# Optimization experiments

Hardware: AMD Instinct MI355X
Metric: run time of the kernel (lower is better)

Reference implementation:

```python
import jax, jax.numpy as jnp
import numpy as np

N_NODES = 100000
N_EDGES = 600000
N_GRAPHS = 64
EPS = 1e-5


def setup_inputs() -> dict:
    key = jax.random.key(0)
    ks = jax.random.split(key, 8)
    x = jax.random.normal(ks[0], (N_NODES, 128), dtype=jnp.float32)
    edge_index = jax.random.randint(ks[1], (2, N_EDGES), 0, N_NODES, dtype=jnp.int64)
    batch = jnp.sort(jax.random.randint(ks[2], (N_NODES,), 0, N_GRAPHS, dtype=jnp.int64))
    conv_w = jax.random.normal(ks[3], (6, 128, 128), dtype=jnp.float32) * (1.0 / np.sqrt(128))
    conv_b = jnp.zeros((6, 128), dtype=jnp.float32)
    bn_g = jnp.ones((6, 128), dtype=jnp.float32)
    bn_b = jnp.zeros((6, 128), dtype=jnp.float32)
    lin1_w = jax.random.normal(ks[4], (128, 64), dtype=jnp.float32) * (1.0 / np.sqrt(128))
    lin1_b = jnp.zeros((64,), dtype=jnp.float32)
    lin2_w = jax.random.normal(ks[5], (64, 4), dtype=jnp.float32) * (1.0 / np.sqrt(64))
    lin2_b = jnp.zeros((4,), dtype=jnp.float32)
    return {"x": x, "edge_index": edge_index, "batch": batch,
            "conv_w": conv_w, "conv_b": conv_b, "bn_g": bn_g, "bn_b": bn_b,
            "lin1_w": lin1_w, "lin1_b": lin1_b, "lin2_w": lin2_w, "lin2_b": lin2_b}


def reference(x, edge_index, batch, conv_w, conv_b, bn_g, bn_b, lin1_w, lin1_b, lin2_w, lin2_b):
    src, dst = edge_index[0], edge_index[1]  # messages flow src -> dst (PyG source_to_target)
    n = x.shape[0]
    h = x
    # 6 stacked GCNConv(normalize=False) -> ReLU -> BatchNorm1d (training-mode batch stats)
    for i in range(6):
        m = h @ conv_w[i]                                   # [N, H] transform first
        agg = jax.ops.segment_sum(m[src], dst, num_segments=n) + conv_b[i]
        h = jax.nn.relu(agg)
        mean = h.mean(axis=0)
        var = h.var(axis=0)                                  # biased, matches torch BN
        h = (h - mean) * jax.lax.rsqrt(var + EPS) * bn_g[i] + bn_b[i]
    # global mean pool over graphs
    s = jax.ops.segment_sum(h, batch, num_segments=N_GRAPHS)          # [G, H]
    cnt = jax.ops.segment_sum(jnp.ones((n,), h.dtype), batch, num_segments=N_GRAPHS)
    pooled = s / jnp.maximum(cnt, 1.0)[:, None]
    out = pooled @ lin1_w + lin1_b
    out = out @ lin2_w + lin2_b
    return jax.nn.log_softmax(out, axis=-1)
```

## Files before the change

kernel.cpp:

```cpp
#include <hip/hip_runtime.h>
#include <math.h>

#define NN 100000
#define NE 600000
#define NG 64
#define HD 128
#define NL 6
#define NB 1563
#define PSL 16
#define ASTR 136

typedef unsigned short ushort_t;
typedef short short8 __attribute__((ext_vector_type(8)));
typedef float floatx4 __attribute__((ext_vector_type(4)));

__device__ __forceinline__ float bf2f(ushort_t u) {
    return __uint_as_float(((unsigned)u) << 16);
}
__device__ __forceinline__ ushort_t f2bf(float f) {
    unsigned u = __float_as_uint(f);
    unsigned r = (u + 0x7fffu + ((u >> 16) & 1u)) >> 16;
    return (ushort_t)r;
}


__global__ __launch_bounds__(256) void k_cast(const float* __restrict__ x,
                                              ushort_t* __restrict__ xb) {
    int i = blockIdx.x * 256 + threadIdx.x;
    if (i < NN * 32) {
        float4 v = ((const float4*)x)[i];
        ((ushort4*)xb)[i] = make_ushort4(f2bf(v.x), f2bf(v.y), f2bf(v.z), f2bf(v.w));
    }
}


__global__ __launch_bounds__(256) void k_wcast(const float* __restrict__ W,
                                               ushort_t* __restrict__ Wt) {
    const float* Wl = W + blockIdx.x * 16384;
    ushort_t* Wtl = Wt + blockIdx.x * 16384;
    for (int id = threadIdx.x; id < 16384; id += 256) {
        int k = id >> 7, c = id & 127;
        Wtl[c * 128 + k] = f2bf(Wl[id]);
    }
}


__global__ __launch_bounds__(256) void k_hist(const int* __restrict__ ei, int* __restrict__ counts) {
    int e = blockIdx.x * 256 + threadIdx.x;
    if (e < NE) atomicAdd(&counts[ei[NE + e]], 1);
}

__global__ __launch_bounds__(256) void k_scan1(const int* __restrict__ counts, int* __restrict__ bsums) {
    __shared__ int s[256];
    int i = blockIdx.x * 256 + threadIdx.x;
    s[threadIdx.x] = (i < NN) ? counts[i] : 0;
    __syncthreads();
    for (int off = 128; off > 0; off >>= 1) {
        if (threadIdx.x < off) s[threadIdx.x] += s[threadIdx.x + off];
        __syncthreads();
    }
    if (threadIdx.x == 0) bsums[blockIdx.x] = s[0];
}

__global__ __launch_bounds__(512) void k_scan2(int* __restrict__ bsums, int nb) {
    __shared__ int s[512];
    int t = threadIdx.x;
    s[t] = (t < nb) ? bsums[t] : 0;
    __syncthreads();
    for (int off = 1; off < 512; off <<= 1) {
        int v = (t >= off) ? s[t - off] : 0;
        __syncthreads();
        s[t] += v;
        __syncthreads();
    }
    if (t < nb) bsums[t] = (t == 0) ? 0 : s[t - 1];
}

__global__ __launch_bounds__(256) void k_scan3(const int* __restrict__ counts, const int* __restrict__ bsums,
                                               int* __restrict__ rowptr) {
    __shared__ int s[256];
    int t = threadIdx.x;
    int i = blockIdx.x * 256 + t;
    int v = (i < NN) ? counts[i] : 0;
    s[t] = v;
    __syncthreads();
    for (int off = 1; off < 256; off <<= 1) {
        int u = (t >= off) ? s[t - off] : 0;
        __syncthreads();
        s[t] += u;
        __syncthreads();
    }
    if (i < NN) rowptr[i] = bsums[blockIdx.x] + s[t] - v;
    if (i == 0) rowptr[NN] = NE;
}

__global__ __launch_bounds__(256) void k_fill(const int* __restrict__ ei, const int* __restrict__ rowptr,
                                              int* __restrict__ cursor, int* __restrict__ colsrc) {
    int e = blockIdx.x * 256 + threadIdx.x;
    if (e < NE) {
        int d = ei[NE + e];
        int pos = rowptr[d] + atomicAdd(&cursor[d], 1);
        colsrc[pos] = ei[e];
    }
}


__global__ __launch_bounds__(256) void k_dhist(const int* __restrict__ rowptr,
                                               int* __restrict__ dcount) {
    __shared__ int lc[64];
    int t = threadIdx.x;
    if (t < 64) lc[t] = 0;
    __syncthreads();
    int n = blockIdx.x * 256 + t;
    if (n < NN) {
        int d = rowptr[n + 1] - rowptr[n];
        atomicAdd(&lc[min(d, 63)], 1);
    }
    __syncthreads();
    if (t < 64 && lc[t] > 0) atomicAdd(&dcount[t], lc[t]);
}

__global__ __launch_bounds__(64) void k_dscan(const int* __restrict__ dcount,
                                              int* __restrict__ doff) {
    int t = threadIdx.x;
    int s = 0;
    for (int b = t + 1; b < 64; ++b) s += dcount[b];
    doff[t] = s;
}

__global__ __launch_bounds__(256) void k_dfill(const int* __restrict__ rowptr,
                                               const int* __restrict__ doff,
                                               int* __restrict__ dcursor,
                                               int* __restrict__ perm) {
    __shared__ int lc[64], lbase[64];
    int t = threadIdx.x;
    if (t < 64) lc[t] = 0;
    __syncthreads();
    int n = blockIdx.x * 256 + t;
    int b = 0, my = 0;
    if (n < NN) {
        int d = rowptr[n + 1] - rowptr[n];
        b = min(d, 63);
        my = atomicAdd(&lc[b], 1);
    }
    __syncthreads();
    if (t < 64 && lc[t] > 0) lbase[t] = atomicAdd(&dcursor[t], lc[t]);
    __syncthreads();
    if (n < NN) perm[doff[b] + lbase[b] + my] = n;
}


__global__ __launch_bounds__(256, 4) void k_gconv(
    const ushort_t* __restrict__ hin, const int* __restrict__ perm,
    const int* __restrict__ rowptr, const int* __restrict__ colsrc,
    const float* __restrict__ stats, const float* __restrict__ bng,
    const float* __restrict__ bnb,
    const ushort_t* __restrict__ Wt, const float* __restrict__ bias,
    ushort_t* __restrict__ hout, float* __restrict__ partials) {
    __shared__ ushort_t Ab[64 * ASTR];
    __shared__ float sstat[256];
    int t = threadIdx.x;
    sstat[t] = 0.f;
    int wave = t >> 6, lane = t & 63;
    int l15 = lane & 15, quad = lane >> 4;
    int rowbase = blockIdx.x * 64 + wave * 16;

    float sc0 = 1.f, sc1 = 1.f, sh0 = 0.f, sh1 = 0.f;
    {
        int c0 = lane * 2;
        if (stats != nullptr) {
            const float inv_n = 1.0f / (float)NN;
            float m0 = stats[c0] * inv_n, m1 = stats[c0 + 1] * inv_n;
            float var0 = fmaf(-m0, m0, stats[HD + c0] * inv_n);
            float var1 = fmaf(-m1, m1, stats[HD + c0 + 1] * inv_n);
            sc0 = bng[c0] * rsqrtf(var0 + 1e-5f);
            sc1 = bng[c0 + 1] * rsqrtf(var1 + 1e-5f);
            sh0 = bnb[c0] - m0 * sc0;
            sh1 = bnb[c0 + 1] - m1 * sc1;
        }
    }

    const ushort2* h2 = (const ushort2*)hin;
    #pragma unroll 1
    for (int g = 0; g < 4; ++g) {
        int b[4], d[4];
        #pragma unroll
        for (int i = 0; i < 4; ++i) {
            int idx = rowbase + g * 4 + i;
            bool v = idx < NN;
            int r = v ? perm[idx] : 0;
            b[i] = v ? rowptr[r] : 0;
            int e2 = v ? rowptr[r + 1] : 0;
            d[i] = e2 - b[i];
        }
        int maxd = max(max(d[0], d[1]), max(d[2], d[3]));
        float ax[4] = {0.f, 0.f, 0.f, 0.f};
        float ay[4] = {0.f, 0.f, 0.f, 0.f};

        int cs[16];
        #pragma unroll
        for (int eo = 0; eo < 4; ++eo)
            #pragma unroll
            for (int i = 0; i < 4; ++i)
                cs[eo * 4 + i] = colsrc[(eo < d[i]) ? b[i] + eo : 0];

        #pragma unroll 1
        for (int e = 0; e < maxd; e += 4) {
            ushort2 hv[16];
            #pragma unroll
            for (int u2 = 0; u2 < 16; ++u2)
                hv[u2] = h2[(size_t)cs[u2] * 64 + lane];
            int ncs[16];
            #pragma unroll
            for (int eo = 0; eo < 4; ++eo)
                #pragma unroll
                for (int i = 0; i < 4; ++i) {
                    int ee = e + 4 + eo;
                    ncs[eo * 4 + i] = colsrc[(ee < d[i]) ? b[i] + ee : 0];
                }
            #pragma unroll
            for (int eo = 0; eo < 4; ++eo)
                #pragma unroll
                for (int i = 0; i < 4; ++i) {
                    float m = (e + eo < d[i]) ? 1.f : 0.f;
                    ushort2 v = hv[eo * 4 + i];
                    ax[i] = fmaf(m, bf2f(v.x), ax[i]);
                    ay[i] = fmaf(m, bf2f(v.y), ay[i]);
                }
            #pragma unroll
            for (int u2 = 0; u2 < 16; ++u2) cs[u2] = ncs[u2];
        }

        #pragma unroll
        for (int i = 0; i < 4; ++i) {
            float degf = (float)d[i];
            float ox = fmaf(sc0, ax[i], degf * sh0);
            float oy = fmaf(sc1, ay[i], degf * sh1);
            int r = wave * 16 + g * 4 + i;
            *(ushort2*)&Ab[r * ASTR + 2 * lane] = make_ushort2(f2bf(ox), f2bf(oy));
        }
    }
    __syncthreads();

    short8 afrag[4];
    #pragma unroll
    for (int s = 0; s < 4; ++s)
        afrag[s] = *(const short8*)&Ab[(wave * 16 + l15) * ASTR + quad * 8 + s * 32];

    floatx4 acc[8];
    #pragma unroll
    for (int c = 0; c < 8; ++c) acc[c] = (floatx4){0.f, 0.f, 0.f, 0.f};
    #pragma unroll
    for (int c = 0; c < 8; ++c) {
        size_t boff = (size_t)(16 * c + l15) * 128 + quad * 8;
        #pragma unroll
        for (int s = 0; s < 4; ++s) {
            short8 bf = *(const short8*)(Wt + boff + 32 * s);
            acc[c] = __builtin_amdgcn_mfma_f32_16x16x32_bf16(afrag[s], bf, acc[c], 0, 0, 0);
        }
    }

    int orow0 = rowbase + quad * 4;
    #pragma unroll
    for (int c = 0; c < 8; ++c) {
        int col = 16 * c + l15;
        float bv = bias[col];
        float ls = 0.f, lq = 0.f;
        #pragma unroll
        for (int i = 0; i < 4; ++i) {
            float v = fmaxf(acc[c][i] + bv, 0.f);
            ushort_t bb = f2bf(v);
            Ab[(wave * 16 + quad * 4 + i) * ASTR + col] = bb;
            if (orow0 + i < NN) {
                float vr = bf2f(bb);
                ls += vr;
                lq = fmaf(vr, vr, lq);
            }
        }
        ls += __shfl_xor(ls, 16, 64);
        ls += __shfl_xor(ls, 32, 64);
        lq += __shfl_xor(lq, 16, 64);
        lq += __shfl_xor(lq, 32, 64);
        if (quad == 0) {
            atomicAdd(&sstat[col], ls);
            atomicAdd(&sstat[128 + col], lq);
        }
    }

    #pragma unroll
    for (int it = 0; it < 4; ++it) {
        int ridx = rowbase + it * 4 + quad;
        if (ridx < NN) {
            int pr = perm[ridx];
            short8 v = *(const short8*)&Ab[(wave * 16 + it * 4 + quad) * ASTR + l15 * 8];
            *(short8*)(hout + (size_t)pr * 128 + l15 * 8) = v;
        }
    }

    __syncthreads();
    partials[(size_t)blockIdx.x * 256 + t] = sstat[t];
}


__global__ __launch_bounds__(256) void k_red(const float* __restrict__ partials,
                                             float* __restrict__ stats) {
    int t = threadIdx.x;
    float s = 0.f;
    for (int r = blockIdx.x; r < NB; r += 64) s += partials[(size_t)r * 256 + t];
    atomicAdd(&stats[t], s);
}


__device__ __forceinline__ int lowerb(const int* __restrict__ b, int n, int key) {
    int lo = 0, hi = n;
    while (lo < hi) {
        int mid = (lo + hi) >> 1;
        if (b[mid] < key) lo = mid + 1;
        else hi = mid;
    }
    return lo;
}

__global__ __launch_bounds__(256) void k_pool1(
    const ushort_t* __restrict__ h, const int* __restrict__ batch,
    float* __restrict__ ppart) {
    int g = blockIdx.x >> 4;
    int sl = blockIdx.x & (PSL - 1);
    int lo = lowerb(batch, NN, g);
    int hi = lowerb(batch, NN, g + 1);
    int cnt = hi - lo;
    int a = lo + (int)(((long long)cnt * sl) >> 4);
    int b = lo + (int)(((long long)cnt * (sl + 1)) >> 4);
    int wave = threadIdx.x >> 6, lane = threadIdx.x & 63;
    const ushort2* h2 = (const ushort2*)h;
    float ax = 0.f, ay = 0.f;
    for (int n = a + wave; n < b; n += 4) {
        ushort2 v = h2[(size_t)n * 64 + lane];
        ax += bf2f(v.x);
        ay += bf2f(v.y);
    }
    __shared__ float2 red[4][64];
    red[wave][lane] = make_float2(ax, ay);
    __syncthreads();
    if (wave == 0) {
        float sx = 0.f, sy = 0.f;
        for (int w = 0; w < 4; ++w) {
            sx += red[w][lane].x;
            sy += red[w][lane].y;
        }
        ((float2*)ppart)[(size_t)blockIdx.x * 64 + lane] = make_float2(sx, sy);
    }
}


__global__ __launch_bounds__(64) void k_pool2(
    const float* __restrict__ ppart, const int* __restrict__ batch,
    const float* __restrict__ stats, const float* __restrict__ bng, const float* __restrict__ bnb,
    float* __restrict__ pooled) {
    int g = blockIdx.x;
    int lane = threadIdx.x;
    float sx = 0.f, sy = 0.f;
    #pragma unroll
    for (int s = 0; s < PSL; ++s) {
        float2 v = ((const float2*)ppart)[(size_t)(g * PSL + s) * 64 + lane];
        sx += v.x;
        sy += v.y;
    }
    int cnt = lowerb(batch, NN, g + 1) - lowerb(batch, NN, g);
    int c0 = lane * 2;
    const float inv_n = 1.0f / (float)NN;
    float m0 = stats[c0] * inv_n, m1 = stats[c0 + 1] * inv_n;
    float var0 = fmaf(-m0, m0, stats[HD + c0] * inv_n);
    float var1 = fmaf(-m1, m1, stats[HD + c0 + 1] * inv_n);
    float sc0 = bng[c0] * rsqrtf(var0 + 1e-5f);
    float sc1 = bng[c0 + 1] * rsqrtf(var1 + 1e-5f);
    float sh0 = bnb[c0] - m0 * sc0;
    float sh1 = bnb[c0 + 1] - m1 * sc1;
    float denom = fmaxf((float)cnt, 1.f);
    float2 o;
    o.x = (sc0 * sx + (float)cnt * sh0) / denom;
    o.y = (sc1 * sy + (float)cnt * sh1) / denom;
    ((float2*)pooled)[g * 64 + lane] = o;
}


__global__ __launch_bounds__(64) void k_head(
    const float* __restrict__ pooled, const float* __restrict__ w1, const float* __restrict__ b1,
    const float* __restrict__ w2, const float* __restrict__ b2, float* __restrict__ out) {
    int g = blockIdx.x;
    int j = threadIdx.x;
    float hid = b1[j];
    const float* p = pooled + g * 128;
    #pragma unroll 8
    for (int k = 0; k < 128; ++k) hid = fmaf(p[k], w1[k * 64 + j], hid);
    float o[4];
    #pragma unroll
    for (int c = 0; c < 4; ++c) {
        float v = hid * w2[j * 4 + c];
        #pragma unroll
        for (int off = 1; off < 64; off <<= 1) v += __shfl_xor(v, off, 64);
        o[c] = v + b2[c];
    }
    if (j == 0) {
        float mx = fmaxf(fmaxf(o[0], o[1]), fmaxf(o[2], o[3]));
        float se = expf(o[0] - mx) + expf(o[1] - mx) + expf(o[2] - mx) + expf(o[3] - mx);
        float ls = mx + logf(se);
        #pragma unroll
        for (int c = 0; c < 4; ++c) out[g * 4 + c] = o[c] - ls;
    }
}

extern "C" void kernel_launch(void* const* d_in, const int* in_sizes, int n_in,
                              void* d_out, int out_size, void* d_ws, size_t ws_size,
                              hipStream_t stream) {
    const float* x = (const float*)d_in[0];
    const int* ei = (const int*)d_in[1];
    const int* batch = (const int*)d_in[2];
    const float* conv_w = (const float*)d_in[3];
    const float* conv_b = (const float*)d_in[4];
    const float* bn_g = (const float*)d_in[5];
    const float* bn_b = (const float*)d_in[6];
    const float* l1w = (const float*)d_in[7];
    const float* l1b = (const float*)d_in[8];
    const float* l2w = (const float*)d_in[9];
    const float* l2b = (const float*)d_in[10];
    float* out = (float*)d_out;
    (void)in_sizes; (void)n_in; (void)out_size; (void)ws_size;

    char* ws = (char*)d_ws;
    int* counts = (int*)(ws + 0);
    int* dcount = (int*)(ws + 0);
    int* dcursor = (int*)(ws + 256);
    int* doff = (int*)(ws + 512);
    int* cursor = (int*)(ws + 400000);
    int* perm = (int*)(ws + 400000);
    float* stats = (float*)(ws + 800000);
    const size_t zero_bytes = 806144;
    int* rowptr = (int*)(ws + 806144);
    int* bsums = (int*)(ws + 1206400);
    int* colsrc = (int*)(ws + 1208192);
    float* pooled = (float*)(ws + 3608192);
    float* ppart = (float*)(ws + 3641344);
    float* partials = (float*)(ws + 4165632);
    ushort_t* xb = (ushort_t*)(ws + 5766656);
    ushort_t* hb0 = (ushort_t*)(ws + 31366656);
    ushort_t* hb1 = (ushort_t*)(ws + 56966656);
    ushort_t* wtbuf = (ushort_t*)(ws + 82566656);

    hipMemsetAsync(ws, 0, zero_bytes, stream);

    k_cast<<<(NN * 32 + 255) / 256, 256, 0, stream>>>(x, xb);
    k_wcast<<<NL, 256, 0, stream>>>(conv_w, wtbuf);

    int ebl = (NE + 255) / 256;
    int nb1 = (NN + 255) / 256;
    k_hist<<<ebl, 256, 0, stream>>>(ei, counts);
    k_scan1<<<nb1, 256, 0, stream>>>(counts, bsums);
    k_scan2<<<1, 512, 0, stream>>>(bsums, nb1);
    k_scan3<<<nb1, 256, 0, stream>>>(counts, bsums, rowptr);
    k_fill<<<ebl, 256, 0, stream>>>(ei, rowptr, cursor, colsrc);

    hipMemsetAsync(ws, 0, 512, stream);
    k_dhist<<<nb1, 256, 0, stream>>>(rowptr, dcount);
    k_dscan<<<1, 64, 0, stream>>>(dcount, doff);
    k_dfill<<<nb1, 256, 0, stream>>>(rowptr, doff, dcursor, perm);

    ushort_t* hb[2] = {hb0, hb1};
    for (int L = 0; L < NL; ++L) {
        const ushort_t* hin = (L == 0) ? xb : hb[(L + 1) & 1];
        ushort_t* hout = hb[L & 1];
        const float* lstats = (L == 0) ? nullptr : (stats + (L - 1) * 256);
        const float* lg = (L == 0) ? nullptr : (bn_g + (L - 1) * 128);
        const float* lb = (L == 0) ? nullptr : (bn_b + (L - 1) * 128);
        k_gconv<<<NB, 256, 0, stream>>>(hin, perm, rowptr, colsrc, lstats, lg, lb,
                                        wtbuf + L * 16384, conv_b + L * 128,
                                        hout, partials);
        k_red<<<64, 256, 0, stream>>>(partials, stats + L * 256);
    }
    k_pool1<<<NG * PSL, 256, 0, stream>>>(hb1, batch, ppart);
    k_pool2<<<NG, 64, 0, stream>>>(ppart, batch, stats + 5 * 256, bn_g + 5 * 128, bn_b + 5 * 128, pooled);
    k_head<<<NG, 64, 0, stream>>>(pooled, l1w, l1b, l2w, l2b, out);
}
```

Baseline: 694.8 us.

## Restructure gather to half-wave rows, fuse preprocessing and tail kernels

The aggregation loop in the graph conv kernel now has each half-wave gather one destination row with 8-byte loads, two rows per pass. It drops per-edge masking by pointing padded edges at a zero sentinel row NN, and prefetches column indices for the next group. Separately, cast with weight transpose, scan stages, fill with degree histogram, degree scan with fill, and pool2 with head are each fused into single launches, cutting launch count and a memset. The sentinel relies on rows past NN in the bf16 buffers being zeroed, which adds workspace layout assumptions.

```diff
diff --git a/kernel.cpp b/kernel.cpp
--- a/kernel.cpp
+++ b/kernel.cpp
@@ -9,6 +9,7 @@
 #define NB 1563
 #define PSL 16
 #define ASTR 136
+#define CASTB 12500
 
 typedef unsigned short ushort_t;
 typedef short short8 __attribute__((ext_vector_type(8)));
@@ -24,23 +25,29 @@
 }
 
 
-__global__ __launch_bounds__(256) void k_cast(const float* __restrict__ x,
-                                              ushort_t* __restrict__ xb) {
-    int i = blockIdx.x * 256 + threadIdx.x;
-    if (i < NN * 32) {
+__global__ __launch_bounds__(256) void k_prep(const float* __restrict__ x,
+                                              ushort_t* __restrict__ xb,
+                                              const float* __restrict__ W,
+                                              ushort_t* __restrict__ Wt,
+                                              ushort_t* __restrict__ hb0,
+                                              ushort_t* __restrict__ hb1) {
+    if (blockIdx.x < CASTB) {
+        int i = blockIdx.x * 256 + threadIdx.x;
         float4 v = ((const float4*)x)[i];
         ((ushort4*)xb)[i] = make_ushort4(f2bf(v.x), f2bf(v.y), f2bf(v.z), f2bf(v.w));
-    }
-}
-
-
-__global__ __launch_bounds__(256) void k_wcast(const float* __restrict__ W,
-                                               ushort_t* __restrict__ Wt) {
-    const float* Wl = W + blockIdx.x * 16384;
-    ushort_t* Wtl = Wt + blockIdx.x * 16384;
-    for (int id = threadIdx.x; id < 16384; id += 256) {
-        int k = id >> 7, c = id & 127;
-        Wtl[c * 128 + k] = f2bf(Wl[id]);
+    } else {
+        const float* Wl = W + (size_t)(blockIdx.x - CASTB) * 16384;
+        ushort_t* Wtl = Wt + (size_t)(blockIdx.x - CASTB) * 16384;
+        for (int id = threadIdx.x; id < 16384; id += 256) {
+            int k = id >> 7, c = id & 127;
+            Wtl[c * 128 + k] = f2bf(Wl[id]);
+        }
+        if (blockIdx.x == CASTB && threadIdx.x < 96) {
+            int t = threadIdx.x;
+            ushort_t* base = (t < 32) ? xb : ((t < 64) ? hb0 : hb1);
+            *(ushort4*)(base + (size_t)NN * 128 + (size_t)(t & 31) * 4) =
+                make_ushort4(0, 0, 0, 0);
+        }
     }
 }
 
@@ -62,22 +69,9 @@
     if (threadIdx.x == 0) bsums[blockIdx.x] = s[0];
 }
 
-__global__ __launch_bounds__(512) void k_scan2(int* __restrict__ bsums, int nb) {
-    __shared__ int s[512];
-    int t = threadIdx.x;
-    s[t] = (t < nb) ? bsums[t] : 0;
-    __syncthreads();
-    for (int off = 1; off < 512; off <<= 1) {
-        int v = (t >= off) ? s[t - off] : 0;
-        __syncthreads();
-        s[t] += v;
-        __syncthreads();
-    }
-    if (t < nb) bsums[t] = (t == 0) ? 0 : s[t - 1];
-}
-
-__global__ __launch_bounds__(256) void k_scan3(const int* __restrict__ counts, const int* __restrict__ bsums,
-                                               int* __restrict__ rowptr) {
+__global__ __launch_bounds__(256) void k_scan3m(const int* __restrict__ counts,
+                                                const int* __restrict__ bsums,
+                                                int* __restrict__ rowptr) {
     __shared__ int s[256];
     int t = threadIdx.x;
     int i = blockIdx.x * 256 + t;
@@ -90,51 +84,61 @@
         s[t] += u;
         __syncthreads();
     }
-    if (i < NN) rowptr[i] = bsums[blockIdx.x] + s[t] - v;
+    int incl = s[t];
+    int pb = 0;
+    for (int j = t; j < blockIdx.x; j += 256) pb += bsums[j];
+    __syncthreads();
+    s[t] = pb;
+    __syncthreads();
+    for (int off = 128; off > 0; off >>= 1) {
+        if (t < off) s[t] += s[t + off];
+        __syncthreads();
+    }
+    int base = s[0];
+    if (i < NN) rowptr[i] = base + incl - v;
     if (i == 0) rowptr[NN] = NE;
 }
 
-__global__ __launch_bounds__(256) void k_fill(const int* __restrict__ ei, const int* __restrict__ rowptr,
-                                              int* __restrict__ cursor, int* __restrict__ colsrc) {
-    int e = blockIdx.x * 256 + threadIdx.x;
-    if (e < NE) {
-        int d = ei[NE + e];
-        int pos = rowptr[d] + atomicAdd(&cursor[d], 1);
-        colsrc[pos] = ei[e];
-    }
-}
-
-
-__global__ __launch_bounds__(256) void k_dhist(const int* __restrict__ rowptr,
-                                               int* __restrict__ dcount) {
-    __shared__ int lc[64];
+__global__ __launch_bounds__(256) void k_filldh(const int* __restrict__ ei,
+                                                const int* __restrict__ rowptr,
+                                                int* __restrict__ cursor,
+                                                int* __restrict__ colsrc,
+                                                int* __restrict__ dcount,
+                                                int ebl) {
     int t = threadIdx.x;
-    if (t < 64) lc[t] = 0;
-    __syncthreads();
-    int n = blockIdx.x * 256 + t;
-    if (n < NN) {
-        int d = rowptr[n + 1] - rowptr[n];
-        atomicAdd(&lc[min(d, 63)], 1);
-    }
-    __syncthreads();
-    if (t < 64 && lc[t] > 0) atomicAdd(&dcount[t], lc[t]);
-}
-
-__global__ __launch_bounds__(64) void k_dscan(const int* __restrict__ dcount,
-                                              int* __restrict__ doff) {
+    if ((int)blockIdx.x < ebl) {
+        int e = blockIdx.x * 256 + t;
+        if (e < NE) {
+            int d = ei[NE + e];
+            int pos = rowptr[d] + atomicAdd(&cursor[d], 1);
+            colsrc[pos] = ei[e];
+        }
+    } else {
+        __shared__ int lc[64];
+        if (t < 64) lc[t] = 0;
+        __syncthreads();
+        int n = (blockIdx.x - ebl) * 256 + t;
+        if (n < NN) {
+            int d = rowptr[n + 1] - rowptr[n];
+            atomicAdd(&lc[min(d, 63)], 1);
+        }
+        __syncthreads();
+        if (t < 64 && lc[t] > 0) atomicAdd(&dcount[t], lc[t]);
+    }
+}
+
+__global__ __launch_bounds__(256) void k_dfill2(const int* __restrict__ rowptr,
+                                                const int* __restrict__ dcount,
+                                                int* __restrict__ dcursor,
+                                                int* __restrict__ perm) {
+    __shared__ int lc[64], lbase[64], doffs[64];
     int t = threadIdx.x;
-    int s = 0;
-    for (int b = t + 1; b < 64; ++b) s += dcount[b];
-    doff[t] = s;
-}
-
-__global__ __launch_bounds__(256) void k_dfill(const int* __restrict__ rowptr,
-                                               const int* __restrict__ doff,
-                                               int* __restrict__ dcursor,
-                                               int* __restrict__ perm) {
-    __shared__ int lc[64], lbase[64];
-    int t = threadIdx.x;
-    if (t < 64) lc[t] = 0;
+    if (t < 64) {
+        lc[t] = 0;
+        int s = 0;
+        for (int b = t + 1; b < 64; ++b) s += dcount[b];
+        doffs[t] = s;
+    }
     __syncthreads();
     int n = blockIdx.x * 256 + t;
     int b = 0, my = 0;
@@ -146,7 +150,7 @@
     __syncthreads();
     if (t < 64 && lc[t] > 0) lbase[t] = atomicAdd(&dcursor[t], lc[t]);
     __syncthreads();
-    if (n < NN) perm[doff[b] + lbase[b] + my] = n;
+    if (n < NN) perm[doffs[b] + lbase[b] + my] = n;
 }
 
 
@@ -163,82 +167,121 @@
     sstat[t] = 0.f;
     int wave = t >> 6, lane = t & 63;
     int l15 = lane & 15, quad = lane >> 4;
+    int l5 = lane & 31, half = lane >> 5;
     int rowbase = blockIdx.x * 64 + wave * 16;
 
-    float sc0 = 1.f, sc1 = 1.f, sh0 = 0.f, sh1 = 0.f;
-    {
-        int c0 = lane * 2;
-        if (stats != nullptr) {
-            const float inv_n = 1.0f / (float)NN;
-            float m0 = stats[c0] * inv_n, m1 = stats[c0 + 1] * inv_n;
-            float var0 = fmaf(-m0, m0, stats[HD + c0] * inv_n);
-            float var1 = fmaf(-m1, m1, stats[HD + c0 + 1] * inv_n);
-            sc0 = bng[c0] * rsqrtf(var0 + 1e-5f);
-            sc1 = bng[c0 + 1] * rsqrtf(var1 + 1e-5f);
-            sh0 = bnb[c0] - m0 * sc0;
-            sh1 = bnb[c0 + 1] - m1 * sc1;
-        }
-    }
-
-    const ushort2* h2 = (const ushort2*)hin;
+    int idxg = rowbase + l15;
+    bool vr = idxg < NN;
+    int prm = vr ? perm[idxg] : 0;
+    int rb = vr ? rowptr[prm] : 0;
+    int re = vr ? rowptr[prm + 1] : 0;
+    int dg = re - rb;
+
+    int f0 = l5 * 4;
+    float sc[4] = {1.f, 1.f, 1.f, 1.f}, sh[4] = {0.f, 0.f, 0.f, 0.f};
+    if (stats != nullptr) {
+        const float inv_n = 1.0f / (float)NN;
+        float4 s1 = *(const float4*)&stats[f0];
+        float4 s2 = *(const float4*)&stats[HD + f0];
+        float4 g4 = *(const float4*)&bng[f0];
+        float4 b4 = *(const float4*)&bnb[f0];
+        float m, var;
+        m = s1.x * inv_n; var = fmaf(-m, m, s2.x * inv_n);
+        sc[0] = g4.x * rsqrtf(var + 1e-5f); sh[0] = b4.x - m * sc[0];
+        m = s1.y * inv_n; var = fmaf(-m, m, s2.y * inv_n);
+        sc[1] = g4.y * rsqrtf(var + 1e-5f); sh[1] = b4.y - m * sc[1];
+        m = s1.z * inv_n; var = fmaf(-m, m, s2.z * inv_n);
+        sc[2] = g4.z * rsqrtf(var + 1e-5f); sh[2] = b4.z - m * sc[2];
+        m = s1.w * inv_n; var = fmaf(-m, m, s2.w * inv_n);
+        sc[3] = g4.w * rsqrtf(var + 1e-5f); sh[3] = b4.w - m * sc[3];
+    }
+
+    const uint2* hbl = (const uint2*)hin + l5;
+
+    int b0 = __shfl(rb, half, 64);
+    int d0 = __shfl(dg, half, 64);
+    int b1 = __shfl(rb, 2 + half, 64);
+    int d1 = __shfl(dg, 2 + half, 64);
+    int cs0[4], cs1[4];
+    #pragma unroll
+    for (int eo = 0; eo < 4; ++eo) {
+        int c0 = colsrc[b0 + eo];
+        int c1 = colsrc[b1 + eo];
+        cs0[eo] = (eo < d0) ? c0 : NN;
+        cs1[eo] = (eo < d1) ? c1 : NN;
+    }
+
     #pragma unroll 1
     for (int g = 0; g < 4; ++g) {
-        int b[4], d[4];
-        #pragma unroll
-        for (int i = 0; i < 4; ++i) {
-            int idx = rowbase + g * 4 + i;
-            bool v = idx < NN;
-            int r = v ? perm[idx] : 0;
-            b[i] = v ? rowptr[r] : 0;
-            int e2 = v ? rowptr[r + 1] : 0;
-            d[i] = e2 - b[i];
-        }
-        int maxd = max(max(d[0], d[1]), max(d[2], d[3]));
-        float ax[4] = {0.f, 0.f, 0.f, 0.f};
-        float ay[4] = {0.f, 0.f, 0.f, 0.f};
-
-        int cs[16];
-        #pragma unroll
-        for (int eo = 0; eo < 4; ++eo)
+        int mx = max(d0, d1);
+        mx = max(mx, __shfl_xor(mx, 32, 64));
+
+        float a0[4] = {0.f, 0.f, 0.f, 0.f};
+        float a1[4] = {0.f, 0.f, 0.f, 0.f};
+
+        #pragma unroll 1
+        for (int e = 0; e < mx; e += 4) {
+            uint2 hv0[4], hv1[4];
             #pragma unroll
-            for (int i = 0; i < 4; ++i)
-                cs[eo * 4 + i] = colsrc[(eo < d[i]) ? b[i] + eo : 0];
-
-        #pragma unroll 1
-        for (int e = 0; e < maxd; e += 4) {
-            ushort2 hv[16];
+            for (int eo = 0; eo < 4; ++eo) hv0[eo] = hbl[(size_t)cs0[eo] * 32];
             #pragma unroll
-            for (int u2 = 0; u2 < 16; ++u2)
-                hv[u2] = h2[(size_t)cs[u2] * 64 + lane];
-            int ncs[16];
+            for (int eo = 0; eo < 4; ++eo) hv1[eo] = hbl[(size_t)cs1[eo] * 32];
+            int nc0[4], nc1[4];
             #pragma unroll
-            for (int eo = 0; eo < 4; ++eo)
-                #pragma unroll
-                for (int i = 0; i < 4; ++i) {
-                    int ee = e + 4 + eo;
-                    ncs[eo * 4 + i] = colsrc[(ee < d[i]) ? b[i] + ee : 0];
-                }
+            for (int eo = 0; eo < 4; ++eo) {
+                int e4 = e + 4 + eo;
+                int c0 = colsrc[b0 + e4];
+                int c1 = colsrc[b1 + e4];
+                nc0[eo] = (e4 < d0) ? c0 : NN;
+                nc1[eo] = (e4 < d1) ? c1 : NN;
+            }
             #pragma unroll
-            for (int eo = 0; eo < 4; ++eo)
-                #pragma unroll
-                for (int i = 0; i < 4; ++i) {
-                    float m = (e + eo < d[i]) ? 1.f : 0.f;
-                    ushort2 v = hv[eo * 4 + i];
-                    ax[i] = fmaf(m, bf2f(v.x), ax[i]);
-                    ay[i] = fmaf(m, bf2f(v.y), ay[i]);
-                }
+            for (int eo = 0; eo < 4; ++eo) {
+                unsigned wx = hv0[eo].x, wy = hv0[eo].y;
+                a0[0] += __uint_as_float(wx << 16);
+                a0[1] += __uint_as_float(wx & 0xffff0000u);
+                a0[2] += __uint_as_float(wy << 16);
+                a0[3] += __uint_as_float(wy & 0xffff0000u);
+                unsigned zx = hv1[eo].x, zy = hv1[eo].y;
+                a1[0] += __uint_as_float(zx << 16);
+                a1[1] += __uint_as_float(zx & 0xffff0000u);
+                a1[2] += __uint_as_float(zy << 16);
+                a1[3] += __uint_as_float(zy & 0xffff0000u);
+            }
             #pragma unroll
-            for (int u2 = 0; u2 < 16; ++u2) cs[u2] = ncs[u2];
-        }
-
-        #pragma unroll
-        for (int i = 0; i < 4; ++i) {
-            float degf = (float)d[i];
-            float ox = fmaf(sc0, ax[i], degf * sh0);
-            float oy = fmaf(sc1, ay[i], degf * sh1);
-            int r = wave * 16 + g * 4 + i;
-            *(ushort2*)&Ab[r * ASTR + 2 * lane] = make_ushort2(f2bf(ox), f2bf(oy));
-        }
+            for (int eo = 0; eo < 4; ++eo) { cs0[eo] = nc0[eo]; cs1[eo] = nc1[eo]; }
+        }
+
+        int nb0 = 0, nd0 = 0, nb1 = 0, nd1 = 0;
+        if (g < 3) {
+            int t0 = (g + 1) * 4 + half, t1 = t0 + 2;
+            nb0 = __shfl(rb, t0, 64);
+            nd0 = __shfl(dg, t0, 64);
+            nb1 = __shfl(rb, t1, 64);
+            nd1 = __shfl(dg, t1, 64);
+            #pragma unroll
+            for (int eo = 0; eo < 4; ++eo) {
+                int c0 = colsrc[nb0 + eo];
+                int c1 = colsrc[nb1 + eo];
+                cs0[eo] = (eo < nd0) ? c0 : NN;
+                cs1[eo] = (eo < nd1) ? c1 : NN;
+            }
+        }
+
+        float df0 = (float)d0, df1 = (float)d1;
+        ushort4 u0, u1;
+        u0.x = f2bf(fmaf(sc[0], a0[0], df0 * sh[0]));
+        u0.y = f2bf(fmaf(sc[1], a0[1], df0 * sh[1]));
+        u0.z = f2bf(fmaf(sc[2], a0[2], df0 * sh[2]));
+        u0.w = f2bf(fmaf(sc[3], a0[3], df0 * sh[3]));
+        u1.x = f2bf(fmaf(sc[0], a1[0], df1 * sh[0]));
+        u1.y = f2bf(fmaf(sc[1], a1[1], df1 * sh[1]));
+        u1.z = f2bf(fmaf(sc[2], a1[2], df1 * sh[2]));
+        u1.w = f2bf(fmaf(sc[3], a1[3], df1 * sh[3]));
+        *(ushort4*)&Ab[(wave * 16 + g * 4 + half) * ASTR + f0] = u0;
+        *(ushort4*)&Ab[(wave * 16 + g * 4 + 2 + half) * ASTR + f0] = u1;
+
+        b0 = nb0; d0 = nd0; b1 = nb1; d1 = nd1;
     }
     __syncthreads();
 
@@ -272,9 +315,9 @@
             ushort_t bb = f2bf(v);
             Ab[(wave * 16 + quad * 4 + i) * ASTR + col] = bb;
             if (orow0 + i < NN) {
-                float vr = bf2f(bb);
-                ls += vr;
-                lq = fmaf(vr, vr, lq);
+                float vr2 = bf2f(bb);
+                ls += vr2;
+                lq = fmaf(vr2, vr2, lq);
             }
         }
         ls += __shfl_xor(ls, 16, 64);
@@ -289,9 +332,9 @@
 
     #pragma unroll
     for (int it = 0; it < 4; ++it) {
+        int pr = __shfl(prm, it * 4 + quad, 64);
         int ridx = rowbase + it * 4 + quad;
         if (ridx < NN) {
-            int pr = perm[ridx];
             short8 v = *(const short8*)&Ab[(wave * 16 + it * 4 + quad) * ASTR + l15 * 8];
             *(short8*)(hout + (size_t)pr * 128 + l15 * 8) = v;
         }
@@ -353,10 +396,13 @@
 }
 
 
-__global__ __launch_bounds__(64) void k_pool2(
+__global__ __launch_bounds__(64) void k_tail(
     const float* __restrict__ ppart, const int* __restrict__ batch,
     const float* __restrict__ stats, const float* __restrict__ bng, const float* __restrict__ bnb,
-    float* __restrict__ pooled) {
+    const float* __restrict__ w1, const float* __restrict__ b1,
+    const float* __restrict__ w2, const float* __restrict__ b2,
+    float* __restrict__ out) {
+    __shared__ float p[128];
     int g = blockIdx.x;
     int lane = threadIdx.x;
     float sx = 0.f, sy = 0.f;
@@ -377,31 +423,22 @@
     float sh0 = bnb[c0] - m0 * sc0;
     float sh1 = bnb[c0 + 1] - m1 * sc1;
     float denom = fmaxf((float)cnt, 1.f);
-    float2 o;
-    o.x = (sc0 * sx + (float)cnt * sh0) / denom;
-    o.y = (sc1 * sy + (float)cnt * sh1) / denom;
-    ((float2*)pooled)[g * 64 + lane] = o;
-}
-
-
-__global__ __launch_bounds__(64) void k_head(
-    const float* __restrict__ pooled, const float* __restrict__ w1, const float* __restrict__ b1,
-    const float* __restrict__ w2, const float* __restrict__ b2, float* __restrict__ out) {
-    int g = blockIdx.x;
-    int j = threadIdx.x;
-    float hid = b1[j];
-    const float* p = pooled + g * 128;
+    p[c0] = (sc0 * sx + (float)cnt * sh0) / denom;
+    p[c0 + 1] = (sc1 * sy + (float)cnt * sh1) / denom;
+    __syncthreads();
+
+    float hid = b1[lane];
     #pragma unroll 8
-    for (int k = 0; k < 128; ++k) hid = fmaf(p[k], w1[k * 64 + j], hid);
+    for (int k = 0; k < 128; ++k) hid = fmaf(p[k], w1[k * 64 + lane], hid);
     float o[4];
     #pragma unroll
     for (int c = 0; c < 4; ++c) {
-        float v = hid * w2[j * 4 + c];
+        float v = hid * w2[lane * 4 + c];
         #pragma unroll
         for (int off = 1; off < 64; off <<= 1) v += __shfl_xor(v, off, 64);
         o[c] = v + b2[c];
     }
-    if (j == 0) {
+    if (lane == 0) {
         float mx = fmaxf(fmaxf(o[0], o[1]), fmaxf(o[2], o[3]));
         float se = expf(o[0] - mx) + expf(o[1] - mx) + expf(o[2] - mx) + expf(o[3] - mx);
         float ls = mx + logf(se);
@@ -429,41 +466,33 @@
 
     char* ws = (char*)d_ws;
     int* counts = (int*)(ws + 0);
-    int* dcount = (int*)(ws + 0);
-    int* dcursor = (int*)(ws + 256);
-    int* doff = (int*)(ws + 512);
     int* cursor = (int*)(ws + 400000);
     int* perm = (int*)(ws + 400000);
     float* stats = (float*)(ws + 800000);
-    const size_t zero_bytes = 806144;
-    int* rowptr = (int*)(ws + 806144);
-    int* bsums = (int*)(ws + 1206400);
-    int* colsrc = (int*)(ws + 1208192);
-    float* pooled = (float*)(ws + 3608192);
-    float* ppart = (float*)(ws + 3641344);
-    float* partials = (float*)(ws + 4165632);
-    ushort_t* xb = (ushort_t*)(ws + 5766656);
-    ushort_t* hb0 = (ushort_t*)(ws + 31366656);
-    ushort_t* hb1 = (ushort_t*)(ws + 56966656);
-    ushort_t* wtbuf = (ushort_t*)(ws + 82566656);
+    int* dcount = (int*)(ws + 806144);
+    int* dcursor = (int*)(ws + 806400);
+    const size_t zero_bytes = 806656;
+    int* rowptr = (int*)(ws + 806656);
+    int* bsums = (int*)(ws + 1206664);
+    int* colsrc = (int*)(ws + 1208256);
+    float* ppart = (float*)(ws + 3609280);
+    float* partials = (float*)(ws + 4133568);
+    ushort_t* xb = (ushort_t*)(ws + 5734144);
+    ushort_t* hb0 = (ushort_t*)(ws + 31334400);
+    ushort_t* hb1 = (ushort_t*)(ws + 56934656);
+    ushort_t* wtbuf = (ushort_t*)(ws + 82534912);
 
     hipMemsetAsync(ws, 0, zero_bytes, stream);
 
-    k_cast<<<(NN * 32 + 255) / 256, 256, 0, stream>>>(x, xb);
-    k_wcast<<<NL, 256, 0, stream>>>(conv_w, wtbuf);
+    k_prep<<<CASTB + NL, 256, 0, stream>>>(x, xb, conv_w, wtbuf, hb0, hb1);
 
     int ebl = (NE + 255) / 256;
     int nb1 = (NN + 255) / 256;
     k_hist<<<ebl, 256, 0, stream>>>(ei, counts);
     k_scan1<<<nb1, 256, 0, stream>>>(counts, bsums);
-    k_scan2<<<1, 512, 0, stream>>>(bsums, nb1);
-    k_scan3<<<nb1, 256, 0, stream>>>(counts, bsums, rowptr);
-    k_fill<<<ebl, 256, 0, stream>>>(ei, rowptr, cursor, colsrc);
-
-    hipMemsetAsync(ws, 0, 512, stream);
-    k_dhist<<<nb1, 256, 0, stream>>>(rowptr, dcount);
-    k_dscan<<<1, 64, 0, stream>>>(dcount, doff);
-    k_dfill<<<nb1, 256, 0, stream>>>(rowptr, doff, dcursor, perm);
+    k_scan3m<<<nb1, 256, 0, stream>>>(counts, bsums, rowptr);
+    k_filldh<<<ebl + nb1, 256, 0, stream>>>(ei, rowptr, cursor, colsrc, dcount, ebl);
+    k_dfill2<<<nb1, 256, 0, stream>>>(rowptr, dcount, dcursor, perm);
 
     ushort_t* hb[2] = {hb0, hb1};
     for (int L = 0; L < NL; ++L) {
@@ -478,6 +507,6 @@
         k_red<<<64, 256, 0, stream>>>(partials, stats + L * 256);
     }
     k_pool1<<<NG * PSL, 256, 0, stream>>>(hb1, batch, ppart);
-    k_pool2<<<NG, 64, 0, stream>>>(ppart, batch, stats + 5 * 256, bn_g + 5 * 128, bn_b + 5 * 128, pooled);
-    k_head<<<NG, 64, 0, stream>>>(pooled, l1w, l1b, l2w, l2b, out);
-}
+    k_tail<<<NG, 64, 0, stream>>>(ppart, batch, stats + 5 * 256, bn_g + 5 * 128, bn_b + 5 * 128,
+                                  l1w, l1b, l2w, l2b, out);
+}
```

After: 646.0 us. 7.0% less time.
